# Kernel optimization log

Measured on AMD Instinct MI355X. Metric: run time of the kernel, lower is better.

The kernel has to match this reference:

```python
import jax, jax.numpy as jnp
import numpy as np


def setup_inputs() -> dict:
    key = jax.random.key(0)
    k1, k2 = jax.random.split(key)
    B, L, D, Y = 8, 2048, 512, 8192
    x = jax.random.normal(k1, (B, L, D), dtype=jnp.float32)
    # xavier_uniform init for U.weight [Y, D]
    limit = float(np.sqrt(6.0 / (Y + D)))
    U_weight = jax.random.uniform(k2, (Y, D), dtype=jnp.float32, minval=-limit, maxval=limit)
    return {"x": x, "U_weight": U_weight}


def reference(x, U_weight):
    # scores: [B, Y, L] = U_weight [Y,D] @ x^T [B,D,L]
    scores = jnp.einsum("yd,bld->byl", U_weight, x)
    alpha = jax.nn.softmax(scores, axis=2)  # softmax over sequence dim
    # m: [B, Y, D] = alpha @ x
    m = jnp.einsum("byl,bld->byd", alpha, x)
    return m
```

## Files before the change

### kernel.cpp

```cpp
#include <hip/hip_runtime.h>

typedef unsigned short u16;
typedef unsigned int u32;
typedef __attribute__((ext_vector_type(8))) short bf16x8;
typedef __attribute__((ext_vector_type(4))) float f32x4;

__device__ __forceinline__ u16 f2bf(float f) {
  u32 u = __float_as_uint(f);
  u32 r = (u + 0x7FFFu + ((u >> 16) & 1u)) >> 16;
  return (u16)r;
}

__device__ __forceinline__ void gl_lds16(const u16* g, u16* l) {
  __builtin_amdgcn_global_load_lds(
      (const __attribute__((address_space(1))) u32*)g,
      (__attribute__((address_space(3))) u32*)l, 16, 0, 0);
}

__global__ __launch_bounds__(256) void cvt_bf16(const float* __restrict__ src,
                                                u16* __restrict__ dst, int n4) {
  int g = blockIdx.x * 256 + threadIdx.x;
  if (g < n4) {
    float4 v = ((const float4*)src)[g];
    ushort4 o;
    o.x = f2bf(v.x); o.y = f2bf(v.y); o.z = f2bf(v.z); o.w = f2bf(v.w);
    ((ushort4*)dst)[g] = o;
  }
}

__global__ __launch_bounds__(256) void prep_x(const float* __restrict__ x,
                                              u16* __restrict__ Xb,
                                              u16* __restrict__ XT) {
  __shared__ u16 t[32][33];
  const int b = blockIdx.z;
  const int l0 = blockIdx.y * 32;
  const int d0 = blockIdx.x * 32;
  const int j = threadIdx.x & 31;
  const int t5 = threadIdx.x >> 5;
#pragma unroll
  for (int r = 0; r < 4; r++) {
    int i = r * 8 + t5;
    float v = x[((size_t)b * 2048 + l0 + i) * 512 + d0 + j];
    u16 h = f2bf(v);
    t[i][j] = h;
    Xb[((size_t)b * 2048 + l0 + i) * 512 + d0 + j] = h;
  }
  __syncthreads();
#pragma unroll
  for (int r = 0; r < 4; r++) {
    int i = r * 8 + t5;
    XT[((size_t)b * 512 + d0 + i) * 2048 + l0 + j] = t[j][i];
  }
}

__global__ __launch_bounds__(256) void zred(const float* __restrict__ pz,
                                            float* __restrict__ z) {
  const int i = blockIdx.x * 256 + threadIdx.x;
  const int bz = i >> 13, row = i & 8191;
  const float* p = pz + (size_t)bz * 16 * 8192 + row;
  float s = 0.f;
#pragma unroll
  for (int j = 0; j < 16; j++) s += p[(size_t)j * 8192];
  z[i] = s;
}

__global__ __launch_bounds__(256, 4)
void gemm1k(const u16* __restrict__ A, const u16* __restrict__ B,
            u16* __restrict__ P, float* __restrict__ pz, int nt,
            size_t Bb_str, size_t Cb_str, int gx, int gy) {
  __shared__ u16 lds[16384];

  const int nwg = gx * gy * gridDim.z;
  const int orig = blockIdx.x + gx * (blockIdx.y + gy * blockIdx.z);
  const int cpx = nwg >> 3;
  const int nid = (orig & 7) * cpx + (orig >> 3);
  const int bxi = nid % gx;
  const int byi = (nid / gx) % gy;
  const int bzi = nid / (gx * gy);
  const int m0 = byi * 128, n0 = bxi * 128;

  const int tid = threadIdx.x;
  const int l = tid & 63;
  const int w = tid >> 6;
  const int wy = w >> 1, wx = w & 1;

  const int rowS = tid >> 3;
  const int cS = ((tid & 7) << 4) ^ ((rowS & 7) << 4);
  const u16* srcA0 = A + (size_t)(m0 + rowS) * 512 + (cS >> 1);
  const u16* srcB0 = B + (size_t)bzi * Bb_str + (size_t)(n0 + rowS) * 512 + (cS >> 1);
  const size_t rsk = (size_t)32 * 512;

  const int fr = l & 15;
  const int X = (fr & 7) << 4;
  const int kb = (l >> 4) << 4;
  const int swz0 = (kb ^ X) >> 1;
  const int swz1 = ((64 + kb) ^ X) >> 1;
  const int aRow = (wy * 64 + fr) * 64;
  const int bRow = (wx * 64 + fr) * 64;

  f32x4 acc[4][4] = {};

  for (int t = 0; t < nt; ++t) {
#pragma unroll
    for (int j = 0; j < 4; j++) {
      gl_lds16(srcA0 + j * rsk + t * 64, &lds[tid * 8 + j * 2048]);
      gl_lds16(srcB0 + j * rsk + t * 64, &lds[8192 + tid * 8 + j * 2048]);
    }
    __syncthreads();
#pragma unroll
    for (int ks = 0; ks < 2; ks++) {
      const int swz = ks ? swz1 : swz0;
      bf16x8 bfr[4], afr[4];
#pragma unroll
      for (int n = 0; n < 4; n++) bfr[n] = *(const bf16x8*)&lds[8192 + bRow + n * 1024 + swz];
#pragma unroll
      for (int m = 0; m < 4; m++) afr[m] = *(const bf16x8*)&lds[aRow + m * 1024 + swz];
#pragma unroll
      for (int m = 0; m < 4; m++)
#pragma unroll
        for (int n = 0; n < 4; n++)
          acc[m][n] = __builtin_amdgcn_mfma_f32_16x16x32_bf16(
              afr[m], bfr[n], acc[m][n], 0, 0, 0);
    }
    __syncthreads();
  }

  const int rq = (l >> 4) * 4;
  float rsv[4][4];
#pragma unroll
  for (int m = 0; m < 4; m++) {
    const int lr0 = wy * 64 + m * 16 + rq;
    float rs[4] = {0.f, 0.f, 0.f, 0.f};
#pragma unroll
    for (int n = 0; n < 4; n++) {
      const int lc = wx * 64 + n * 16 + fr;
#pragma unroll
      for (int r = 0; r < 4; r++) {
        const float e = __expf(acc[m][n][r]);
        lds[(lr0 + r) * 128 + lc] = f2bf(e);
        rs[r] += e;
      }
    }
#pragma unroll
    for (int r = 0; r < 4; r++) rsv[m][r] = rs[r];
  }
  __syncthreads();
  u16* Pb = P + (size_t)bzi * Cb_str;
#pragma unroll
  for (int k = 0; k < 8; k++) {
    const int row = k * 16 + (tid >> 4);
    const int cu = (tid & 15) * 8;
    *(uint4*)&Pb[(size_t)(m0 + row) * 2048 + n0 + cu] = *(const uint4*)&lds[row * 128 + cu];
  }
  __syncthreads();

  float* pzl = (float*)lds;
#pragma unroll
  for (int m = 0; m < 4; m++)
#pragma unroll
    for (int r = 0; r < 4; r++)
      pzl[(wy * 64 + m * 16 + rq + r) * 33 + wx * 16 + fr] = rsv[m][r];
  __syncthreads();
  {
    const int row = tid >> 1, half = tid & 1;
    float s = 0.f;
#pragma unroll
    for (int j = 0; j < 16; j++) s += pzl[row * 33 + half * 16 + j];
    s += __shfl_xor(s, 1);
    if (!half) pz[((size_t)bzi * 16 + bxi) * 8192 + m0 + row] = s;
  }
}

__global__ __launch_bounds__(512, 4)
void gemm2k(const u16* __restrict__ A, const u16* __restrict__ B,
            float* __restrict__ Cout, const float* __restrict__ z,
            int Kstride, int nt, int N,
            size_t Ab_str, size_t Bb_str, size_t Cb_str, int gx, int gy) {
  __shared__ u16 lds[24576];
  __shared__ float rz_lds[128];

  const int nwg = gx * gy * gridDim.z;
  const int orig = blockIdx.x + gx * (blockIdx.y + gy * blockIdx.z);
  const int cpx = nwg >> 3;
  const int nid = (orig & 7) * cpx + (orig >> 3);
  const int bxi = nid % gx;
  const int byi = (nid / gx) % gy;
  const int bzi = nid / (gx * gy);
  const int m0 = byi * 128, n0 = bxi * 256;

  const u16* Ab = A + (size_t)bzi * Ab_str;
  const u16* Bb = B + (size_t)bzi * Bb_str;

  const int tid = threadIdx.x;
  const int l = tid & 63;
  const int w = tid >> 6;
  const int wm = w >> 2, wn = w & 3;

  const int rowS = tid >> 3;
  const int cS = ((tid & 7) << 4) ^ ((rowS & 7) << 4);
  const u16* srcA0 = Ab + (size_t)(m0 + rowS) * Kstride + (cS >> 1);
  const u16* srcB0 = Bb + (size_t)(n0 + rowS) * Kstride + (cS >> 1);
  const size_t rsk = (size_t)64 * Kstride;

  const int fr = l & 15;
  const int X = (fr & 7) << 4;
  const int kb = (l >> 4) << 4;
  const int swz0 = (kb ^ X) >> 1;
  const int swz1 = ((64 + kb) ^ X) >> 1;
  const int aRow = (wm * 64 + fr) * 64;
  const int bRow = 8192 + (wn * 64 + fr) * 64;

  if (tid < 128) rz_lds[tid] = 1.f / z[(size_t)bzi * 8192 + m0 + tid];

  f32x4 acc[4][4] = {};

  for (int t = 0; t < nt; ++t) {
#pragma unroll
    for (int j = 0; j < 2; j++)
      gl_lds16(srcA0 + j * rsk + t * 64, &lds[tid * 8 + j * 4096]);
#pragma unroll
    for (int j = 0; j < 4; j++)
      gl_lds16(srcB0 + j * rsk + t * 64, &lds[8192 + tid * 8 + j * 4096]);
    __syncthreads();
#pragma unroll
    for (int ks = 0; ks < 2; ks++) {
      const int swz = ks ? swz1 : swz0;
      bf16x8 bfr[4], afr[4];
#pragma unroll
      for (int n = 0; n < 4; n++) bfr[n] = *(const bf16x8*)&lds[bRow + n * 1024 + swz];
#pragma unroll
      for (int m = 0; m < 4; m++) afr[m] = *(const bf16x8*)&lds[aRow + m * 1024 + swz];
#pragma unroll
      for (int m = 0; m < 4; m++)
#pragma unroll
        for (int n = 0; n < 4; n++)
          acc[m][n] = __builtin_amdgcn_mfma_f32_16x16x32_bf16(
              afr[m], bfr[n], acc[m][n], 0, 0, 0);
    }
    __syncthreads();
  }

  const int rq = (l >> 4) * 4;
#pragma unroll
  for (int m = 0; m < 4; m++) {
    const int lrow = wm * 64 + m * 16 + rq;
    const int grow = m0 + lrow;
#pragma unroll
    for (int n = 0; n < 4; n++) {
      const int col = n0 + wn * 64 + n * 16 + fr;
#pragma unroll
      for (int r = 0; r < 4; r++)
        Cout[(size_t)bzi * Cb_str + (size_t)(grow + r) * N + col] =
            acc[m][n][r] * rz_lds[lrow + r];
    }
  }
}

extern "C" void kernel_launch(void* const* d_in, const int* in_sizes, int n_in,
                              void* d_out, int out_size, void* d_ws, size_t ws_size,
                              hipStream_t stream) {
  const float* x = (const float*)d_in[0];
  const float* U = (const float*)d_in[1];
  if (n_in >= 2 && in_sizes[0] == 8192 * 512) {
    x = (const float*)d_in[1];
    U = (const float*)d_in[0];
  }
  float* out = (float*)d_out;
  char* ws = (char*)d_ws;

  u16* Ub = (u16*)ws;
  u16* Xb = (u16*)(ws + 8388608);
  u16* XT = (u16*)(ws + 25165824);
  u16* P  = (u16*)(ws + 41943040);
  float* pz = (float*)(ws + 41943040 + 268435456);
  float* z  = (float*)(ws + 41943040 + 268435456 + 4194304);
  const size_t need_all = 41943040ull + 268435456ull + 4194304ull + 262144ull;

  cvt_bf16<<<4096, 256, 0, stream>>>(U, Ub, (8192 * 512) / 4);
  prep_x<<<dim3(16, 64, 8), 256, 0, stream>>>(x, Xb, XT);

  if (ws_size >= need_all) {
    gemm1k<<<dim3(16, 64, 8), 256, 0, stream>>>(
        Ub, Xb, P, pz, 8, (size_t)2048 * 512, (size_t)8192 * 2048, 16, 64);
    zred<<<256, 256, 0, stream>>>(pz, z);
    gemm2k<<<dim3(2, 64, 8), 512, 0, stream>>>(
        P, XT, out, z, 2048, 32, 512,
        (size_t)8192 * 2048, (size_t)512 * 2048, (size_t)8192 * 512, 2, 64);
  } else {
    u16* Pf = P;
    float* pzf = (float*)(ws + 41943040 + 33554432);
    float* zf = pzf + 16 * 8192;
    for (int b = 0; b < 8; b++) {
      gemm1k<<<dim3(16, 64, 1), 256, 0, stream>>>(
          Ub, Xb + (size_t)b * 2048 * 512, Pf, pzf, 8, 0, 0, 16, 64);
      zred<<<32, 256, 0, stream>>>(pzf, zf);
      gemm2k<<<dim3(2, 64, 1), 512, 0, stream>>>(
          Pf, XT + (size_t)b * 512 * 2048, out + (size_t)b * 8192 * 512,
          zf, 2048, 32, 512, 0, 0, 0, 2, 64);
    }
  }
}
```

Baseline: 341.8 us.

## Widen score GEMM tile to 128x256 with 512 threads and two-pass epilogue

The first GEMM (scores plus exp) now uses a 128x256 output tile per workgroup with 8 waves instead of 128x128 with 4 waves. This halves the number of column tiles and cuts redundant reloads of the U operand. The epilogue writes P in two 128-column halves through the existing LDS buffer, and the partial row-sum buffer shrinks from 16 to 8 column partials, so zred sums fewer terms. The cost is a larger LDS footprint, extra barriers in the epilogue, and fewer workgroups in the grid.

New measurement: 352.0 us. 3.0% more time.

```diff
diff --git a/kernel.cpp b/kernel.cpp
--- a/kernel.cpp
+++ b/kernel.cpp
@@ -57,127 +57,18 @@
                                             float* __restrict__ z) {
   const int i = blockIdx.x * 256 + threadIdx.x;
   const int bz = i >> 13, row = i & 8191;
-  const float* p = pz + (size_t)bz * 16 * 8192 + row;
+  const float* p = pz + (size_t)bz * 8 * 8192 + row;
   float s = 0.f;
 #pragma unroll
-  for (int j = 0; j < 16; j++) s += p[(size_t)j * 8192];
+  for (int j = 0; j < 8; j++) s += p[(size_t)j * 8192];
   z[i] = s;
 }
 
-__global__ __launch_bounds__(256, 4)
+__global__ __launch_bounds__(512, 4)
 void gemm1k(const u16* __restrict__ A, const u16* __restrict__ B,
             u16* __restrict__ P, float* __restrict__ pz, int nt,
             size_t Bb_str, size_t Cb_str, int gx, int gy) {
-  __shared__ u16 lds[16384];
-
-  const int nwg = gx * gy * gridDim.z;
-  const int orig = blockIdx.x + gx * (blockIdx.y + gy * blockIdx.z);
-  const int cpx = nwg >> 3;
-  const int nid = (orig & 7) * cpx + (orig >> 3);
-  const int bxi = nid % gx;
-  const int byi = (nid / gx) % gy;
-  const int bzi = nid / (gx * gy);
-  const int m0 = byi * 128, n0 = bxi * 128;
-
-  const int tid = threadIdx.x;
-  const int l = tid & 63;
-  const int w = tid >> 6;
-  const int wy = w >> 1, wx = w & 1;
-
-  const int rowS = tid >> 3;
-  const int cS = ((tid & 7) << 4) ^ ((rowS & 7) << 4);
-  const u16* srcA0 = A + (size_t)(m0 + rowS) * 512 + (cS >> 1);
-  const u16* srcB0 = B + (size_t)bzi * Bb_str + (size_t)(n0 + rowS) * 512 + (cS >> 1);
-  const size_t rsk = (size_t)32 * 512;
-
-  const int fr = l & 15;
-  const int X = (fr & 7) << 4;
-  const int kb = (l >> 4) << 4;
-  const int swz0 = (kb ^ X) >> 1;
-  const int swz1 = ((64 + kb) ^ X) >> 1;
-  const int aRow = (wy * 64 + fr) * 64;
-  const int bRow = (wx * 64 + fr) * 64;
-
-  f32x4 acc[4][4] = {};
-
-  for (int t = 0; t < nt; ++t) {
-#pragma unroll
-    for (int j = 0; j < 4; j++) {
-      gl_lds16(srcA0 + j * rsk + t * 64, &lds[tid * 8 + j * 2048]);
-      gl_lds16(srcB0 + j * rsk + t * 64, &lds[8192 + tid * 8 + j * 2048]);
-    }
-    __syncthreads();
-#pragma unroll
-    for (int ks = 0; ks < 2; ks++) {
-      const int swz = ks ? swz1 : swz0;
-      bf16x8 bfr[4], afr[4];
-#pragma unroll
-      for (int n = 0; n < 4; n++) bfr[n] = *(const bf16x8*)&lds[8192 + bRow + n * 1024 + swz];
-#pragma unroll
-      for (int m = 0; m < 4; m++) afr[m] = *(const bf16x8*)&lds[aRow + m * 1024 + swz];
-#pragma unroll
-      for (int m = 0; m < 4; m++)
-#pragma unroll
-        for (int n = 0; n < 4; n++)
-          acc[m][n] = __builtin_amdgcn_mfma_f32_16x16x32_bf16(
-              afr[m], bfr[n], acc[m][n], 0, 0, 0);
-    }
-    __syncthreads();
-  }
-
-  const int rq = (l >> 4) * 4;
-  float rsv[4][4];
-#pragma unroll
-  for (int m = 0; m < 4; m++) {
-    const int lr0 = wy * 64 + m * 16 + rq;
-    float rs[4] = {0.f, 0.f, 0.f, 0.f};
-#pragma unroll
-    for (int n = 0; n < 4; n++) {
-      const int lc = wx * 64 + n * 16 + fr;
-#pragma unroll
-      for (int r = 0; r < 4; r++) {
-        const float e = __expf(acc[m][n][r]);
-        lds[(lr0 + r) * 128 + lc] = f2bf(e);
-        rs[r] += e;
-      }
-    }
-#pragma unroll
-    for (int r = 0; r < 4; r++) rsv[m][r] = rs[r];
-  }
-  __syncthreads();
-  u16* Pb = P + (size_t)bzi * Cb_str;
-#pragma unroll
-  for (int k = 0; k < 8; k++) {
-    const int row = k * 16 + (tid >> 4);
-    const int cu = (tid & 15) * 8;
-    *(uint4*)&Pb[(size_t)(m0 + row) * 2048 + n0 + cu] = *(const uint4*)&lds[row * 128 + cu];
-  }
-  __syncthreads();
-
-  float* pzl = (float*)lds;
-#pragma unroll
-  for (int m = 0; m < 4; m++)
-#pragma unroll
-    for (int r = 0; r < 4; r++)
-      pzl[(wy * 64 + m * 16 + rq + r) * 33 + wx * 16 + fr] = rsv[m][r];
-  __syncthreads();
-  {
-    const int row = tid >> 1, half = tid & 1;
-    float s = 0.f;
-#pragma unroll
-    for (int j = 0; j < 16; j++) s += pzl[row * 33 + half * 16 + j];
-    s += __shfl_xor(s, 1);
-    if (!half) pz[((size_t)bzi * 16 + bxi) * 8192 + m0 + row] = s;
-  }
-}
-
-__global__ __launch_bounds__(512, 4)
-void gemm2k(const u16* __restrict__ A, const u16* __restrict__ B,
-            float* __restrict__ Cout, const float* __restrict__ z,
-            int Kstride, int nt, int N,
-            size_t Ab_str, size_t Bb_str, size_t Cb_str, int gx, int gy) {
   __shared__ u16 lds[24576];
-  __shared__ float rz_lds[128];
 
   const int nwg = gx * gy * gridDim.z;
   const int orig = blockIdx.x + gx * (blockIdx.y + gy * blockIdx.z);
@@ -188,6 +79,123 @@
   const int bzi = nid / (gx * gy);
   const int m0 = byi * 128, n0 = bxi * 256;
 
+  const int tid = threadIdx.x;
+  const int l = tid & 63;
+  const int w = tid >> 6;
+  const int wm = w >> 2, wn = w & 3;
+
+  const int rowS = tid >> 3;
+  const int cS = ((tid & 7) << 4) ^ ((rowS & 7) << 4);
+  const u16* srcA0 = A + (size_t)(m0 + rowS) * 512 + (cS >> 1);
+  const u16* srcB0 = B + (size_t)bzi * Bb_str + (size_t)(n0 + rowS) * 512 + (cS >> 1);
+  const size_t rsk = (size_t)64 * 512;
+
+  const int fr = l & 15;
+  const int X = (fr & 7) << 4;
+  const int kb = (l >> 4) << 4;
+  const int swz0 = (kb ^ X) >> 1;
+  const int swz1 = ((64 + kb) ^ X) >> 1;
+  const int aRow = (wm * 64 + fr) * 64;
+  const int bRow = 8192 + (wn * 64 + fr) * 64;
+
+  f32x4 acc[4][4] = {};
+
+  for (int t = 0; t < nt; ++t) {
+#pragma unroll
+    for (int j = 0; j < 2; j++)
+      gl_lds16(srcA0 + j * rsk + t * 64, &lds[tid * 8 + j * 4096]);
+#pragma unroll
+    for (int j = 0; j < 4; j++)
+      gl_lds16(srcB0 + j * rsk + t * 64, &lds[8192 + tid * 8 + j * 4096]);
+    __syncthreads();
+#pragma unroll
+    for (int ks = 0; ks < 2; ks++) {
+      const int swz = ks ? swz1 : swz0;
+      bf16x8 bfr[4], afr[4];
+#pragma unroll
+      for (int n = 0; n < 4; n++) bfr[n] = *(const bf16x8*)&lds[bRow + n * 1024 + swz];
+#pragma unroll
+      for (int m = 0; m < 4; m++) afr[m] = *(const bf16x8*)&lds[aRow + m * 1024 + swz];
+#pragma unroll
+      for (int m = 0; m < 4; m++)
+#pragma unroll
+        for (int n = 0; n < 4; n++)
+          acc[m][n] = __builtin_amdgcn_mfma_f32_16x16x32_bf16(
+              afr[m], bfr[n], acc[m][n], 0, 0, 0);
+    }
+    __syncthreads();
+  }
+
+  const int rq = (l >> 4) * 4;
+  u16* Pb = P + (size_t)bzi * Cb_str;
+  float rsv[4][4];
+#pragma unroll
+  for (int half = 0; half < 2; half++) {
+    if ((wn >> 1) == half) {
+#pragma unroll
+      for (int m = 0; m < 4; m++) {
+        const int lr0 = wm * 64 + m * 16 + rq;
+        float rs[4] = {0.f, 0.f, 0.f, 0.f};
+#pragma unroll
+        for (int n = 0; n < 4; n++) {
+          const int lc = (wn & 1) * 64 + n * 16 + fr;
+#pragma unroll
+          for (int r = 0; r < 4; r++) {
+            const float e = __expf(acc[m][n][r]);
+            lds[(lr0 + r) * 128 + lc] = f2bf(e);
+            rs[r] += e;
+          }
+        }
+#pragma unroll
+        for (int r = 0; r < 4; r++) rsv[m][r] = rs[r];
+      }
+    }
+    __syncthreads();
+#pragma unroll
+    for (int k = 0; k < 4; k++) {
+      const int row = k * 32 + (tid >> 4);
+      const int cu = (tid & 15) * 8;
+      *(uint4*)&Pb[(size_t)(m0 + row) * 2048 + n0 + half * 128 + cu] =
+          *(const uint4*)&lds[row * 128 + cu];
+    }
+    __syncthreads();
+  }
+
+  float* pzl = (float*)lds;
+#pragma unroll
+  for (int m = 0; m < 4; m++)
+#pragma unroll
+    for (int r = 0; r < 4; r++)
+      pzl[(wm * 64 + m * 16 + rq + r) * 65 + wn * 16 + fr] = rsv[m][r];
+  __syncthreads();
+  {
+    const int row = tid >> 2, q = tid & 3;
+    float s = 0.f;
+#pragma unroll
+    for (int j = 0; j < 16; j++) s += pzl[row * 65 + q * 16 + j];
+    s += __shfl_xor(s, 1);
+    s += __shfl_xor(s, 2);
+    if (q == 0) pz[((size_t)bzi * 8 + bxi) * 8192 + m0 + row] = s;
+  }
+}
+
+__global__ __launch_bounds__(512, 4)
+void gemm2k(const u16* __restrict__ A, const u16* __restrict__ B,
+            float* __restrict__ Cout, const float* __restrict__ z,
+            int Kstride, int nt, int N,
+            size_t Ab_str, size_t Bb_str, size_t Cb_str, int gx, int gy) {
+  __shared__ u16 lds[24576];
+  __shared__ float rz_lds[128];
+
+  const int nwg = gx * gy * gridDim.z;
+  const int orig = blockIdx.x + gx * (blockIdx.y + gy * blockIdx.z);
+  const int cpx = nwg >> 3;
+  const int nid = (orig & 7) * cpx + (orig >> 3);
+  const int bxi = nid % gx;
+  const int byi = (nid / gx) % gy;
+  const int bzi = nid / (gx * gy);
+  const int m0 = byi * 128, n0 = bxi * 256;
+
   const u16* Ab = A + (size_t)bzi * Ab_str;
   const u16* Bb = B + (size_t)bzi * Bb_str;
 
@@ -273,15 +281,15 @@
   u16* XT = (u16*)(ws + 25165824);
   u16* P  = (u16*)(ws + 41943040);
   float* pz = (float*)(ws + 41943040 + 268435456);
-  float* z  = (float*)(ws + 41943040 + 268435456 + 4194304);
-  const size_t need_all = 41943040ull + 268435456ull + 4194304ull + 262144ull;
+  float* z  = (float*)(ws + 41943040 + 268435456 + 2097152);
+  const size_t need_all = 41943040ull + 268435456ull + 2097152ull + 262144ull;
 
   cvt_bf16<<<4096, 256, 0, stream>>>(U, Ub, (8192 * 512) / 4);
   prep_x<<<dim3(16, 64, 8), 256, 0, stream>>>(x, Xb, XT);
 
   if (ws_size >= need_all) {
-    gemm1k<<<dim3(16, 64, 8), 256, 0, stream>>>(
-        Ub, Xb, P, pz, 8, (size_t)2048 * 512, (size_t)8192 * 2048, 16, 64);
+    gemm1k<<<dim3(8, 64, 8), 512, 0, stream>>>(
+        Ub, Xb, P, pz, 8, (size_t)2048 * 512, (size_t)8192 * 2048, 8, 64);
     zred<<<256, 256, 0, stream>>>(pz, z);
     gemm2k<<<dim3(2, 64, 8), 512, 0, stream>>>(
         P, XT, out, z, 2048, 32, 512,
@@ -289,10 +297,10 @@
   } else {
     u16* Pf = P;
     float* pzf = (float*)(ws + 41943040 + 33554432);
-    float* zf = pzf + 16 * 8192;
+    float* zf = pzf + 8 * 8192;
     for (int b = 0; b < 8; b++) {
-      gemm1k<<<dim3(16, 64, 1), 256, 0, stream>>>(
-          Ub, Xb + (size_t)b * 2048 * 512, Pf, pzf, 8, 0, 0, 16, 64);
+      gemm1k<<<dim3(8, 64, 1), 512, 0, stream>>>(
+          Ub, Xb + (size_t)b * 2048 * 512, Pf, pzf, 8, 0, 0, 8, 64);
       zred<<<32, 256, 0, stream>>>(pzf, zf);
       gemm2k<<<dim3(2, 64, 1), 512, 0, stream>>>(
           Pf, XT + (size_t)b * 512 * 2048, out + (size_t)b * 8192 * 512,
```
